# Kernel tuning notes

Hardware: AMD Instinct MI355X
Metric: run time of the kernel (lower is better)

## Reference

```python
import jax, jax.numpy as jnp
import numpy as np

DIM = 4096
CAP = 8192
EPS = 1e-8  # torch F.cosine_similarity denominator clamp


def setup_inputs() -> dict:
    key = jax.random.key(0)
    k1, k2, k3, k4, k5, k6 = jax.random.split(key, 6)
    return {
        "query": jax.random.normal(k1, (DIM,), dtype=jnp.float32),
        "memory_bank": jax.random.normal(k2, (CAP, DIM), dtype=jnp.float32),
        "importance": jax.random.uniform(k3, (CAP,), dtype=jnp.float32),
        "age": jax.random.uniform(k4, (CAP,), dtype=jnp.float32) * 1000.0,
        "W_dec": jax.random.normal(k5, (DIM, DIM), dtype=jnp.float32) * (1.0 / np.sqrt(DIM)),
        "b_dec": jax.random.normal(k6, (DIM,), dtype=jnp.float32) * 0.01,
        "top_k": 8,
    }


def reference(query, memory_bank, importance, age, W_dec, b_dec, top_k):
    # Cosine similarity of query against every memory row (torch semantics:
    # dot / max(||q||*||m||, eps)).
    dots = memory_bank @ query                       # [CAP]
    qn = jnp.sqrt(jnp.sum(query * query))
    mn = jnp.sqrt(jnp.sum(memory_bank * memory_bank, axis=1))
    sim = dots / jnp.maximum(qn * mn, EPS)
    # Time-decayed importance weighting.
    weighted = sim * importance * jnp.exp(-0.001 * age)
    # Top-k retrieval, mean-pool retrieved rows, decode.
    _, idx = jax.lax.top_k(weighted, top_k)          # [k]
    retrieved = jnp.mean(memory_bank[idx], axis=0)   # [DIM]
    return retrieved @ W_dec.T + b_dec
```

## Files before the change

### kernel.cpp

```cpp
#include <hip/hip_runtime.h>
#include <math.h>

#define DIM 4096
#define CAP 8192
#define EPS 1e-8f

__global__ __launch_bounds__(256) void score_kernel(
    const float* __restrict__ q,
    const float* __restrict__ mb,
    const float* __restrict__ imp,
    const float* __restrict__ age,
    float* __restrict__ weighted)
{
    const int row = blockIdx.x;
    const float4* __restrict__ mrow = (const float4*)(mb + (size_t)row * DIM);
    const float4* __restrict__ q4   = (const float4*)q;

    float dot = 0.f, msq = 0.f, qsq = 0.f;
    for (int i = threadIdx.x; i < DIM / 4; i += 256) {
        float4 m  = mrow[i];
        float4 qq = q4[i];
        dot += m.x * qq.x + m.y * qq.y + m.z * qq.z + m.w * qq.w;
        msq += m.x * m.x + m.y * m.y + m.z * m.z + m.w * m.w;
        qsq += qq.x * qq.x + qq.y * qq.y + qq.z * qq.z + qq.w * qq.w;
    }

    for (int off = 32; off > 0; off >>= 1) {
        dot += __shfl_down(dot, off, 64);
        msq += __shfl_down(msq, off, 64);
        qsq += __shfl_down(qsq, off, 64);
    }

    __shared__ float sdot[4], smsq[4], sqsq[4];
    const int wave = threadIdx.x >> 6;
    const int lane = threadIdx.x & 63;
    if (lane == 0) { sdot[wave] = dot; smsq[wave] = msq; sqsq[wave] = qsq; }
    __syncthreads();

    if (threadIdx.x == 0) {
        float d = 0.f, ms = 0.f, qs = 0.f;
        for (int w = 0; w < 4; ++w) { d += sdot[w]; ms += smsq[w]; qs += sqsq[w]; }
        float denom = fmaxf(sqrtf(qs) * sqrtf(ms), EPS);
        weighted[row] = (d / denom) * imp[row] * expf(-0.001f * age[row]);
    }
}

__global__ __launch_bounds__(1024) void topk_gather_kernel(
    const float* __restrict__ weighted,
    const float* __restrict__ mb,
    const int* __restrict__ topk_ptr,
    float* __restrict__ retrieved)
{
    __shared__ float wv[CAP];
    __shared__ float rv[16];
    __shared__ int   ri[16];
    __shared__ int   sidx[64];

    const int tid = threadIdx.x;
    for (int i = tid; i < CAP; i += 1024) wv[i] = weighted[i];
    __syncthreads();

    int k = *topk_ptr;
    if (k < 1) k = 1;
    if (k > 64) k = 64;

    for (int it = 0; it < k; ++it) {
        float bv = -INFINITY; int bi = 0x7fffffff;
        for (int i = tid; i < CAP; i += 1024) {
            float v = wv[i];
            if (v > bv) { bv = v; bi = i; }
        }
        for (int off = 32; off > 0; off >>= 1) {
            float ov = __shfl_down(bv, off, 64);
            int   oi = __shfl_down(bi, off, 64);
            if (ov > bv || (ov == bv && oi < bi)) { bv = ov; bi = oi; }
        }
        const int wave = tid >> 6;
        const int lane = tid & 63;
        if (lane == 0) { rv[wave] = bv; ri[wave] = bi; }
        __syncthreads();
        if (tid == 0) {
            float best = rv[0]; int besti = ri[0];
            for (int w = 1; w < 16; ++w) {
                if (rv[w] > best || (rv[w] == best && ri[w] < besti)) {
                    best = rv[w]; besti = ri[w];
                }
            }
            sidx[it] = besti;
            wv[besti] = -INFINITY;
        }
        __syncthreads();
    }

    const float inv_k = 1.0f / (float)k;
    for (int i = tid; i < DIM / 4; i += 1024) {
        float4 acc = make_float4(0.f, 0.f, 0.f, 0.f);
        for (int r = 0; r < k; ++r) {
            const float4* __restrict__ row = (const float4*)(mb + (size_t)sidx[r] * DIM);
            float4 v = row[i];
            acc.x += v.x; acc.y += v.y; acc.z += v.z; acc.w += v.w;
        }
        acc.x *= inv_k; acc.y *= inv_k; acc.z *= inv_k; acc.w *= inv_k;
        ((float4*)retrieved)[i] = acc;
    }
}

__global__ __launch_bounds__(256) void decode_kernel(
    const float* __restrict__ W,
    const float* __restrict__ b,
    const float* __restrict__ r,
    float* __restrict__ out)
{
    const int j = blockIdx.x;
    const float4* __restrict__ wrow = (const float4*)(W + (size_t)j * DIM);
    const float4* __restrict__ r4   = (const float4*)r;

    float acc = 0.f;
    for (int i = threadIdx.x; i < DIM / 4; i += 256) {
        float4 w = wrow[i];
        float4 v = r4[i];
        acc += w.x * v.x + w.y * v.y + w.z * v.z + w.w * v.w;
    }
    for (int off = 32; off > 0; off >>= 1) acc += __shfl_down(acc, off, 64);

    __shared__ float sacc[4];
    const int wave = threadIdx.x >> 6;
    const int lane = threadIdx.x & 63;
    if (lane == 0) sacc[wave] = acc;
    __syncthreads();
    if (threadIdx.x == 0) {
        float s = sacc[0] + sacc[1] + sacc[2] + sacc[3];
        out[j] = s + b[j];
    }
}

extern "C" void kernel_launch(void* const* d_in, const int* in_sizes, int n_in,
                              void* d_out, int out_size, void* d_ws, size_t ws_size,
                              hipStream_t stream) {
    const float* query      = (const float*)d_in[0];
    const float* memory     = (const float*)d_in[1];
    const float* importance = (const float*)d_in[2];
    const float* age        = (const float*)d_in[3];
    const float* W_dec      = (const float*)d_in[4];
    const float* b_dec      = (const float*)d_in[5];
    const int*   top_k      = (const int*)d_in[6];

    float* weighted  = (float*)d_ws;
    float* retrieved = (float*)d_ws + CAP;
    float* out       = (float*)d_out;

    score_kernel<<<CAP, 256, 0, stream>>>(query, memory, importance, age, weighted);
    topk_gather_kernel<<<1, 1024, 0, stream>>>(weighted, memory, top_k, retrieved);
    decode_kernel<<<DIM, 256, 0, stream>>>(W_dec, b_dec, retrieved, out);
}
```

Before: 262.8 us.

## Use one wave per row in score/decode and incremental per-thread top-k rescans

Score and decode kernels now assign one 64-lane wave per row instead of a 256-thread block per row, which removes the shared-memory reduction and block barrier, and their inner loops are unrolled with explicit FMAs. The top-k kernel drops to 512 threads and keeps each thread's local maximum across iterations. Only the thread that owned the selected element rescans its 16 strided slots, so the k full passes over 8192 shared values are avoided. The trade-off is longer per-lane loops with fewer threads per row.

Measured after the change: 260.2 us. Within noise of the previous version (-1.0%).

```diff
diff --git a/kernel.cpp b/kernel.cpp
--- a/kernel.cpp
+++ b/kernel.cpp
@@ -12,76 +12,83 @@
     const float* __restrict__ age,
     float* __restrict__ weighted)
 {
-    const int row = blockIdx.x;
+    const int wave = threadIdx.x >> 6;
+    const int lane = threadIdx.x & 63;
+    const int row  = (blockIdx.x << 2) + wave;
+
     const float4* __restrict__ mrow = (const float4*)(mb + (size_t)row * DIM);
     const float4* __restrict__ q4   = (const float4*)q;
 
     float dot = 0.f, msq = 0.f, qsq = 0.f;
-    for (int i = threadIdx.x; i < DIM / 4; i += 256) {
+    #pragma unroll 4
+    for (int i = lane; i < DIM / 4; i += 64) {
         float4 m  = mrow[i];
         float4 qq = q4[i];
-        dot += m.x * qq.x + m.y * qq.y + m.z * qq.z + m.w * qq.w;
-        msq += m.x * m.x + m.y * m.y + m.z * m.z + m.w * m.w;
-        qsq += qq.x * qq.x + qq.y * qq.y + qq.z * qq.z + qq.w * qq.w;
+        dot = fmaf(m.w, qq.w, fmaf(m.z, qq.z, fmaf(m.y, qq.y, fmaf(m.x, qq.x, dot))));
+        msq = fmaf(m.w, m.w,  fmaf(m.z, m.z,  fmaf(m.y, m.y,  fmaf(m.x, m.x,  msq))));
+        qsq = fmaf(qq.w, qq.w, fmaf(qq.z, qq.z, fmaf(qq.y, qq.y, fmaf(qq.x, qq.x, qsq))));
     }
-
+    #pragma unroll
     for (int off = 32; off > 0; off >>= 1) {
         dot += __shfl_down(dot, off, 64);
         msq += __shfl_down(msq, off, 64);
         qsq += __shfl_down(qsq, off, 64);
     }
-
-    __shared__ float sdot[4], smsq[4], sqsq[4];
-    const int wave = threadIdx.x >> 6;
-    const int lane = threadIdx.x & 63;
-    if (lane == 0) { sdot[wave] = dot; smsq[wave] = msq; sqsq[wave] = qsq; }
-    __syncthreads();
-
-    if (threadIdx.x == 0) {
-        float d = 0.f, ms = 0.f, qs = 0.f;
-        for (int w = 0; w < 4; ++w) { d += sdot[w]; ms += smsq[w]; qs += sqsq[w]; }
-        float denom = fmaxf(sqrtf(qs) * sqrtf(ms), EPS);
-        weighted[row] = (d / denom) * imp[row] * expf(-0.001f * age[row]);
+    if (lane == 0) {
+        float denom = fmaxf(sqrtf(qsq) * sqrtf(msq), EPS);
+        weighted[row] = (dot / denom) * imp[row] * expf(-0.001f * age[row]);
     }
 }
 
-__global__ __launch_bounds__(1024) void topk_gather_kernel(
+__global__ __launch_bounds__(512) void topk_gather_kernel(
     const float* __restrict__ weighted,
     const float* __restrict__ mb,
     const int* __restrict__ topk_ptr,
     float* __restrict__ retrieved)
 {
     __shared__ float wv[CAP];
-    __shared__ float rv[16];
-    __shared__ int   ri[16];
+    __shared__ float rv[8];
+    __shared__ int   ri[8];
     __shared__ int   sidx[64];
 
-    const int tid = threadIdx.x;
-    for (int i = tid; i < CAP; i += 1024) wv[i] = weighted[i];
+    const int tid  = threadIdx.x;
+    const int wave = tid >> 6;
+    const int lane = tid & 63;
+
+    {
+        const float4* __restrict__ w4  = (const float4*)weighted;
+        float4* __restrict__       wv4 = (float4*)wv;
+        #pragma unroll
+        for (int i = tid; i < CAP / 4; i += 512) wv4[i] = w4[i];
+    }
     __syncthreads();
 
     int k = *topk_ptr;
     if (k < 1) k = 1;
     if (k > 64) k = 64;
 
+    float bv = -INFINITY; int bi = tid;
+    #pragma unroll
+    for (int j = 0; j < CAP / 512; ++j) {
+        const int idx = tid + (j << 9);
+        const float v = wv[idx];
+        if (v > bv) { bv = v; bi = idx; }
+    }
+
     for (int it = 0; it < k; ++it) {
-        float bv = -INFINITY; int bi = 0x7fffffff;
-        for (int i = tid; i < CAP; i += 1024) {
-            float v = wv[i];
-            if (v > bv) { bv = v; bi = i; }
+        float cv = bv; int ci = bi;
+        #pragma unroll
+        for (int off = 32; off > 0; off >>= 1) {
+            float ov = __shfl_down(cv, off, 64);
+            int   oi = __shfl_down(ci, off, 64);
+            if (ov > cv || (ov == cv && oi < ci)) { cv = ov; ci = oi; }
         }
-        for (int off = 32; off > 0; off >>= 1) {
-            float ov = __shfl_down(bv, off, 64);
-            int   oi = __shfl_down(bi, off, 64);
-            if (ov > bv || (ov == bv && oi < bi)) { bv = ov; bi = oi; }
-        }
-        const int wave = tid >> 6;
-        const int lane = tid & 63;
-        if (lane == 0) { rv[wave] = bv; ri[wave] = bi; }
+        if (lane == 0) { rv[wave] = cv; ri[wave] = ci; }
         __syncthreads();
         if (tid == 0) {
             float best = rv[0]; int besti = ri[0];
-            for (int w = 1; w < 16; ++w) {
+            #pragma unroll
+            for (int w = 1; w < 8; ++w) {
                 if (rv[w] > best || (rv[w] == best && ri[w] < besti)) {
                     best = rv[w]; besti = ri[w];
                 }
@@ -90,14 +97,24 @@
             wv[besti] = -INFINITY;
         }
         __syncthreads();
+        const int gbi = sidx[it];
+        if ((gbi & 511) == tid) {
+            bv = -INFINITY; bi = tid;
+            #pragma unroll
+            for (int j = 0; j < CAP / 512; ++j) {
+                const int idx = tid + (j << 9);
+                const float v = wv[idx];
+                if (v > bv) { bv = v; bi = idx; }
+            }
+        }
     }
+    __syncthreads();
 
     const float inv_k = 1.0f / (float)k;
-    for (int i = tid; i < DIM / 4; i += 1024) {
+    for (int i = tid; i < DIM / 4; i += 512) {
         float4 acc = make_float4(0.f, 0.f, 0.f, 0.f);
         for (int r = 0; r < k; ++r) {
-            const float4* __restrict__ row = (const float4*)(mb + (size_t)sidx[r] * DIM);
-            float4 v = row[i];
+            const float4 v = ((const float4*)(mb + (size_t)sidx[r] * DIM))[i];
             acc.x += v.x; acc.y += v.y; acc.z += v.z; acc.w += v.w;
         }
         acc.x *= inv_k; acc.y *= inv_k; acc.z *= inv_k; acc.w *= inv_k;
@@ -111,27 +128,23 @@
     const float* __restrict__ r,
     float* __restrict__ out)
 {
-    const int j = blockIdx.x;
+    const int wave = threadIdx.x >> 6;
+    const int lane = threadIdx.x & 63;
+    const int j    = (blockIdx.x << 2) + wave;
+
     const float4* __restrict__ wrow = (const float4*)(W + (size_t)j * DIM);
     const float4* __restrict__ r4   = (const float4*)r;
 
     float acc = 0.f;
-    for (int i = threadIdx.x; i < DIM / 4; i += 256) {
+    #pragma unroll 4
+    for (int i = lane; i < DIM / 4; i += 64) {
         float4 w = wrow[i];
         float4 v = r4[i];
-        acc += w.x * v.x + w.y * v.y + w.z * v.z + w.w * v.w;
+        acc = fmaf(w.w, v.w, fmaf(w.z, v.z, fmaf(w.y, v.y, fmaf(w.x, v.x, acc))));
     }
+    #pragma unroll
     for (int off = 32; off > 0; off >>= 1) acc += __shfl_down(acc, off, 64);
-
-    __shared__ float sacc[4];
-    const int wave = threadIdx.x >> 6;
-    const int lane = threadIdx.x & 63;
-    if (lane == 0) sacc[wave] = acc;
-    __syncthreads();
-    if (threadIdx.x == 0) {
-        float s = sacc[0] + sacc[1] + sacc[2] + sacc[3];
-        out[j] = s + b[j];
-    }
+    if (lane == 0) out[j] = acc + b[j];
 }
 
 extern "C" void kernel_launch(void* const* d_in, const int* in_sizes, int n_in,
@@ -149,7 +162,7 @@
     float* retrieved = (float*)d_ws + CAP;
     float* out       = (float*)d_out;
 
-    score_kernel<<<CAP, 256, 0, stream>>>(query, memory, importance, age, weighted);
-    topk_gather_kernel<<<1, 1024, 0, stream>>>(weighted, memory, top_k, retrieved);
-    decode_kernel<<<DIM, 256, 0, stream>>>(W_dec, b_dec, retrieved, out);
+    score_kernel<<<CAP / 4, 256, 0, stream>>>(query, memory, importance, age, weighted);
+    topk_gather_kernel<<<1, 512, 0, stream>>>(weighted, memory, top_k, retrieved);
+    decode_kernel<<<DIM / 4, 256, 0, stream>>>(W_dec, b_dec, retrieved, out);
 }
```
